# Kernel optimization log

Hardware: AMD Instinct MI355X
Metric: run time of the kernel (lower is better)

## Reference

```python
import jax, jax.numpy as jnp
import numpy as np

N = 50000      # nodes
E = 400000     # edges
IN = 64        # in_channels
HID = 64       # hidden_channels
H = 4          # num_heads
LAT = 32       # latent_dim
NEG_SLOPE = 0.2


def setup_inputs() -> dict:
    key = jax.random.key(0)
    ks = jax.random.split(key, 20)
    w = lambda k, shape, s=0.05: (jax.random.normal(k, shape, jnp.float32) * s)
    inp = {
        'x': jax.random.normal(ks[0], (N, IN), jnp.float32),
        'edge_index': jax.random.randint(ks[1], (2, E), 0, N, dtype=jnp.int32),
        'batch': jnp.zeros((N,), jnp.int32),
        'eps': jax.random.normal(ks[2], (N, LAT), jnp.float32),
        # conv1: in -> HID per head, 4 heads, concat
        'W1': w(ks[3], (IN, H * HID)), 'a_src1': w(ks[4], (H, HID)), 'a_dst1': w(ks[5], (H, HID)), 'b1': jnp.zeros((H * HID,), jnp.float32),
        # conv2: H*HID -> HID per head, concat
        'W2': w(ks[6], (H * HID, H * HID)), 'a_src2': w(ks[7], (H, HID)), 'a_dst2': w(ks[8], (H, HID)), 'b2': jnp.zeros((H * HID,), jnp.float32),
        # conv_mu / conv_logvar: H*HID -> LAT, 1 head, no concat
        'Wmu': w(ks[9], (H * HID, LAT)), 'a_src_mu': w(ks[10], (1, LAT)), 'a_dst_mu': w(ks[11], (1, LAT)), 'b_mu': jnp.zeros((LAT,), jnp.float32),
        'Wlv': w(ks[12], (H * HID, LAT)), 'a_src_lv': w(ks[13], (1, LAT)), 'a_dst_lv': w(ks[14], (1, LAT)), 'b_lv': jnp.zeros((LAT,), jnp.float32),
        # decoder
        'W_fc': w(ks[15], (LAT, HID)), 'b_fc': jnp.zeros((HID,), jnp.float32),
        'W_node': w(ks[16], (HID, IN)), 'b_node': jnp.zeros((IN,), jnp.float32),
        'W_edge': w(ks[17], (HID, 1)), 'b_edge': jnp.zeros((1,), jnp.float32),
    }
    return inp


def gat_layer(x, W, a_src, a_dst, b, src, dst, concat):
    """PyG-style GATConv: gather -> leaky_relu score -> per-dst softmax -> scatter-add."""
    n = x.shape[0]
    heads, c = a_src.shape
    h = (x @ W).reshape(n, heads, c)                     # [N,H,C]
    s_src = jnp.einsum('nhc,hc->nh', h, a_src)           # [N,H]
    s_dst = jnp.einsum('nhc,hc->nh', h, a_dst)
    e = jax.nn.leaky_relu(s_src[src] + s_dst[dst], NEG_SLOPE)   # [E,H]
    m = jax.ops.segment_max(e, dst, num_segments=n)      # stable softmax per destination
    e = jnp.exp(e - m[dst])
    denom = jax.ops.segment_sum(e, dst, num_segments=n)
    alpha = e / (denom[dst] + 1e-16)                     # [E,H]
    out = jax.ops.segment_sum(alpha[:, :, None] * h[src], dst, num_segments=n)  # [N,H,C]
    out = out.reshape(n, heads * c) if concat else out.mean(axis=1)
    return out + b


def reference(x, edge_index, batch, eps,
              W1, a_src1, a_dst1, b1,
              W2, a_src2, a_dst2, b2,
              Wmu, a_src_mu, a_dst_mu, b_mu,
              Wlv, a_src_lv, a_dst_lv, b_lv,
              W_fc, b_fc, W_node, b_node, W_edge, b_edge):
    n = x.shape[0]
    src0, dst0 = edge_index[0], edge_index[1]
    loops = jnp.arange(n, dtype=edge_index.dtype)        # GATConv add_self_loops=True
    src = jnp.concatenate([src0, loops])
    dst = jnp.concatenate([dst0, loops])

    # encode
    h = jax.nn.relu(gat_layer(x, W1, a_src1, a_dst1, b1, src, dst, concat=True))
    h = jax.nn.relu(gat_layer(h, W2, a_src2, a_dst2, b2, src, dst, concat=True))
    mu = gat_layer(h, Wmu, a_src_mu, a_dst_mu, b_mu, src, dst, concat=False)
    logvar = gat_layer(h, Wlv, a_src_lv, a_dst_lv, b_lv, src, dst, concat=False)

    # reparameterize (eps supplied for determinism)
    z = mu + eps * jnp.exp(0.5 * logvar)

    # decode
    zd = jax.nn.relu(z @ W_fc + b_fc)                    # [N,HID]
    node_features = zd @ W_node + b_node                 # [N,IN]
    edge_feat = zd[src0] * zd[dst0]                      # [E,HID]
    edge_scores = (edge_feat @ W_edge + b_edge).squeeze(-1)  # [E]
    return (mu, logvar, z, node_features, edge_scores)
```

## Files before the change

kernel.cpp:

```cpp
#include <hip/hip_runtime.h>
#include <math.h>

#define NEG_SLOPE 0.2f
#define CAP 32

__device__ __forceinline__ float lky(float x){ return x > 0.f ? x : NEG_SLOPE * x; }

__device__ __forceinline__ unsigned short f2bf(float f){
  unsigned int u = __float_as_uint(f);
  unsigned int r = (u + 0x7fffu + ((u >> 16) & 1u)) >> 16;
  return (unsigned short)r;
}
__device__ __forceinline__ float bf2f(unsigned short s){
  return __uint_as_float(((unsigned int)s) << 16);
}
__device__ __forceinline__ void unp8(uint4 v, float* f){
  f[0]=__uint_as_float(v.x<<16); f[1]=__uint_as_float(v.x&0xffff0000u);
  f[2]=__uint_as_float(v.y<<16); f[3]=__uint_as_float(v.y&0xffff0000u);
  f[4]=__uint_as_float(v.z<<16); f[5]=__uint_as_float(v.z&0xffff0000u);
  f[6]=__uint_as_float(v.w<<16); f[7]=__uint_as_float(v.w&0xffff0000u);
}
__device__ __forceinline__ uint4 pack8(const float* o){
  uint4 v;
  v.x = (unsigned)f2bf(o[0]) | ((unsigned)f2bf(o[1])<<16);
  v.y = (unsigned)f2bf(o[2]) | ((unsigned)f2bf(o[3])<<16);
  v.z = (unsigned)f2bf(o[4]) | ((unsigned)f2bf(o[5])<<16);
  v.w = (unsigned)f2bf(o[6]) | ((unsigned)f2bf(o[7])<<16);
  return v;
}

typedef __bf16 bf16x8 __attribute__((ext_vector_type(8)));
typedef float  f32x4  __attribute__((ext_vector_type(4)));
typedef float  f32x2  __attribute__((ext_vector_type(2)));

__device__ __forceinline__ uint2 pk_fp8(const float* f){
  unsigned lo = 0u, hi = 0u;
  lo = __builtin_amdgcn_cvt_pk_fp8_f32(f[0], f[1], (int)lo, false);
  lo = __builtin_amdgcn_cvt_pk_fp8_f32(f[2], f[3], (int)lo, true);
  hi = __builtin_amdgcn_cvt_pk_fp8_f32(f[4], f[5], (int)hi, false);
  hi = __builtin_amdgcn_cvt_pk_fp8_f32(f[6], f[7], (int)hi, true);
  return make_uint2(lo, hi);
}
__device__ __forceinline__ unsigned pk_fp8x4(float f0, float f1, float f2, float f3){
  unsigned u = 0u;
  u = __builtin_amdgcn_cvt_pk_fp8_f32(f0, f1, (int)u, false);
  u = __builtin_amdgcn_cvt_pk_fp8_f32(f2, f3, (int)u, true);
  return u;
}
__device__ __forceinline__ void unpk_fp8(uint2 v, float* f){
  f32x2 a0 = __builtin_amdgcn_cvt_pk_f32_fp8((int)v.x, false);
  f32x2 a1 = __builtin_amdgcn_cvt_pk_f32_fp8((int)v.x, true);
  f32x2 a2 = __builtin_amdgcn_cvt_pk_f32_fp8((int)v.y, false);
  f32x2 a3 = __builtin_amdgcn_cvt_pk_f32_fp8((int)v.y, true);
  f[0]=a0[0]; f[1]=a0[1]; f[2]=a1[0]; f[3]=a1[1];
  f[4]=a2[0]; f[5]=a2[1]; f[6]=a3[0]; f[7]=a3[1];
}

__device__ __forceinline__ void pack_one(const float* Wa, const float* Wb,
                                         int K, int M, int Mhalf,
                                         unsigned short* out, int idx){
  if (idx >= K * M) return;
  int j = idx & 7;
  int l = (idx >> 3) & 63;
  int rest = idx >> 9;
  int KS = K >> 5;
  int s = rest % KS, gct = rest / KS;
  int col = gct * 16 + (l & 15);
  int k   = s * 32 + ((l >> 4) << 3) + j;
  float v;
  if (Wb == nullptr) v = Wa[(long)k * M + col];
  else v = (col < Mhalf) ? Wa[(long)k * Mhalf + col] : Wb[(long)k * Mhalf + (col - Mhalf)];
  out[idx] = f2bf(v);
}

__global__ __launch_bounds__(256) void mega_kernel(
    const int* __restrict__ srcA, const int* __restrict__ dstA,
    int* __restrict__ cnt, int* __restrict__ colv2d, int E, int nbE,
    const float* __restrict__ W1,  unsigned short* __restrict__ W1pk,
    const float* __restrict__ W2,  unsigned short* __restrict__ W2pk,
    const float* __restrict__ Wmu, const float* __restrict__ Wlv,
    unsigned short* __restrict__ Wmvpk,
    const float* __restrict__ Wfc, unsigned short* __restrict__ Wfcpk,
    const float* __restrict__ Wnd, unsigned short* __restrict__ Wndpk,
    const float* __restrict__ as1, const float* __restrict__ ad1,
    const float* __restrict__ x, unsigned short* __restrict__ xb,
    float* __restrict__ S1s, float* __restrict__ S1d, int n)
{
  int b = blockIdx.x, t = threadIdx.x;
  if (b < nbE){
    int e = b * 256 + t;
    if (e < E){
      int d = dstA[e];
      int pos = atomicAdd(&cnt[d], 1);
      if (pos < CAP) colv2d[(long)d * CAP + pos] = srcA[e];
    }
    return;
  }
  b -= nbE;
  if (b < 408){
    if (b < 64)       pack_one(W1, nullptr, 64, 256, 256, W1pk, b * 256 + t);
    else if (b < 320) pack_one(W2, nullptr, 256, 256, 256, W2pk, (b - 64) * 256 + t);
    else if (b < 384) pack_one(Wmu, Wlv, 256, 64, 32, Wmvpk, (b - 320) * 256 + t);
    else if (b < 392) pack_one(Wfc, nullptr, 32, 64, 64, Wfcpk, (b - 384) * 256 + t);
    else              pack_one(Wnd, nullptr, 64, 64, 64, Wndpk, (b - 392) * 256 + t);
    return;
  }
  b -= 408;
  __shared__ float PT[512];
  #pragma unroll
  for (int rep = 0; rep < 2; ++rep){
    int idx = t + rep * 256;
    int o = idx >> 6, k = idx & 63;
    int sd = o & 1, h = o >> 1;
    const float* av = sd ? ad1 : as1;
    float acc = 0.f;
    for (int c = 0; c < 64; ++c) acc += W1[k * 256 + h * 64 + c] * av[h * 64 + c];
    PT[idx] = acc;
  }

  long base64 = (long)b * 64;
  {
    const float4* xg = (const float4*)x;
    uint4* xw = (uint4*)xb;
    long lim = (long)n * 8;
    long g0 = base64 * 8;
    #pragma unroll
    for (int rep = 0; rep < 2; ++rep){
      long p = g0 + t + rep * 256;
      if (p < lim){
        float4 v0 = xg[2 * p], v1 = xg[2 * p + 1];
        uint4 o;
        o.x = (unsigned)f2bf(v0.x) | ((unsigned)f2bf(v0.y) << 16);
        o.y = (unsigned)f2bf(v0.z) | ((unsigned)f2bf(v0.w) << 16);
        o.z = (unsigned)f2bf(v1.x) | ((unsigned)f2bf(v1.y) << 16);
        o.w = (unsigned)f2bf(v1.z) | ((unsigned)f2bf(v1.w) << 16);
        xw[p] = o;
      }
    }
  }
  __syncthreads();

  {
    int r = t >> 2, kq = t & 3;
    long nid = base64 + r;
    float acc[8] = {0,0,0,0,0,0,0,0};
    if (nid < n){
      const float4* xr4 = (const float4*)(x + nid * 64 + kq * 16);
      #pragma unroll
      for (int j4 = 0; j4 < 4; ++j4){
        float4 v = xr4[j4];
        float vf[4] = {v.x, v.y, v.z, v.w};
        #pragma unroll
        for (int jj = 0; jj < 4; ++jj){
          int k = kq * 16 + j4 * 4 + jj;
          #pragma unroll
          for (int o = 0; o < 8; ++o) acc[o] += vf[jj] * PT[o * 64 + k];
        }
      }
    }
    #pragma unroll
    for (int o = 0; o < 8; ++o){
      acc[o] += __shfl_xor(acc[o], 1);
      acc[o] += __shfl_xor(acc[o], 2);
    }
    if (kq == 0 && nid < n){
      *(float4*)(S1s + nid * 4) = make_float4(acc[0], acc[2], acc[4], acc[6]);
      *(float4*)(S1d + nid * 4) = make_float4(acc[1], acc[3], acc[5], acc[7]);
    }
  }
}

__global__ __launch_bounds__(256) void aggx_kernel(
    const unsigned short* __restrict__ xb,
    const float* __restrict__ Ss, const float* __restrict__ Sd,
    const int* __restrict__ cnt, const int* __restrict__ colv2d,
    unsigned short* __restrict__ Xagg, int n)
{
  int wv = threadIdx.x >> 6, l = threadIdx.x & 63;
  int nid = blockIdx.x * 4 + wv;
  if (nid >= n) return;
  int slot = l >> 4;
  int cl = l & 15;
  float4 sdv = *(const float4*)(Sd + (long)nid * 4);
  const uint2* xb2 = (const uint2*)xb;
  float acc[4][4] = {};
  float sumw[4] = {0.f, 0.f, 0.f, 0.f};
  int c = cnt[nid]; if (c > CAP) c = CAP;
  long rb = (long)nid * CAP;
  for (int jj = slot; jj < c; jj += 4){
    int s = colv2d[rb + jj];
    float4 a = *(const float4*)(Ss + (long)s * 4);
    float wx = __expf(lky(a.x + sdv.x));
    float wy = __expf(lky(a.y + sdv.y));
    float wz = __expf(lky(a.z + sdv.z));
    float ww = __expf(lky(a.w + sdv.w));
    uint2 xv = xb2[(long)s * 16 + cl];
    float f0 = __uint_as_float(xv.x << 16);
    float f1 = __uint_as_float(xv.x & 0xffff0000u);
    float f2 = __uint_as_float(xv.y << 16);
    float f3 = __uint_as_float(xv.y & 0xffff0000u);
    acc[0][0] += wx*f0; acc[0][1] += wx*f1; acc[0][2] += wx*f2; acc[0][3] += wx*f3;
    acc[1][0] += wy*f0; acc[1][1] += wy*f1; acc[1][2] += wy*f2; acc[1][3] += wy*f3;
    acc[2][0] += wz*f0; acc[2][1] += wz*f1; acc[2][2] += wz*f2; acc[2][3] += wz*f3;
    acc[3][0] += ww*f0; acc[3][1] += ww*f1; acc[3][2] += ww*f2; acc[3][3] += ww*f3;
    sumw[0] += wx; sumw[1] += wy; sumw[2] += wz; sumw[3] += ww;
  }
  #pragma unroll
  for (int d = 16; d <= 32; d <<= 1){
    #pragma unroll
    for (int h = 0; h < 4; ++h){
      #pragma unroll
      for (int j = 0; j < 4; ++j) acc[h][j] += __shfl_xor(acc[h][j], d);
      sumw[h] += __shfl_xor(sumw[h], d);
    }
  }
  float4 ssv = *(const float4*)(Ss + (long)nid * 4);
  uint2 xv = xb2[(long)nid * 16 + cl];
  float f0 = __uint_as_float(xv.x << 16);
  float f1 = __uint_as_float(xv.x & 0xffff0000u);
  float f2 = __uint_as_float(xv.y << 16);
  float f3 = __uint_as_float(xv.y & 0xffff0000u);
  float wsh[4] = { __expf(lky(ssv.x + sdv.x)), __expf(lky(ssv.y + sdv.y)),
                   __expf(lky(ssv.z + sdv.z)), __expf(lky(ssv.w + sdv.w)) };
  if (l < 16){
    uint2* Xo = (uint2*)Xagg;
    #pragma unroll
    for (int h = 0; h < 4; ++h){
      float inv = 1.f / (sumw[h] + wsh[h] + 1e-16f);
      float o0 = (acc[h][0] + wsh[h] * f0) * inv;
      float o1 = (acc[h][1] + wsh[h] * f1) * inv;
      float o2 = (acc[h][2] + wsh[h] * f2) * inv;
      float o3 = (acc[h][3] + wsh[h] * f3) * inv;
      uint2 ov;
      ov.x = (unsigned)f2bf(o0) | ((unsigned)f2bf(o1) << 16);
      ov.y = (unsigned)f2bf(o2) | ((unsigned)f2bf(o3) << 16);
      Xo[(long)nid * 64 + h * 16 + cl] = ov;
    }
  }
}

__global__ __launch_bounds__(256) void gemm12_kernel(
    const unsigned short* __restrict__ Xagg,
    const unsigned short* __restrict__ W1pk, const unsigned short* __restrict__ W2pk,
    const float* __restrict__ b1,
    const float* __restrict__ a_s, const float* __restrict__ a_d,
    unsigned char* __restrict__ H8,
    float* __restrict__ Ss, float* __restrict__ Sd, int n)
{
  constexpr int LDA = 264;
  __shared__ unsigned short As[32 * LDA];
  __shared__ unsigned short Bs[32 * LDA];
  const int t = threadIdx.x;
  const int w = t >> 6, l = t & 63;
  const int quad = l >> 4, l15 = l & 15;
  const long base = (long)blockIdx.x * 32;

  {
    const uint4* Xg = (const uint4*)Xagg;
    long g0 = base * 32;
    long lim = (long)n * 32;
    for (int c = t; c < 1024; c += 256){
      int row = c >> 5, kc = c & 31;
      uint4 v = make_uint4(0u, 0u, 0u, 0u);
      if (g0 + c < lim) v = Xg[g0 + c];
      *(uint4*)(As + row * LDA + kc * 8) = v;
    }
  }
  __syncthreads();

  f32x4 acc1[2][4] = {};
  const int abase = w * 64;
  #pragma unroll
  for (int s = 0; s < 2; ++s){
    bf16x8 af0 = *(const bf16x8*)(As + (0  + l15) * LDA + abase + s * 32 + quad * 8);
    bf16x8 af1 = *(const bf16x8*)(As + (16 + l15) * LDA + abase + s * 32 + quad * 8);
    #pragma unroll
    for (int ct = 0; ct < 4; ++ct){
      int gct = w * 4 + ct;
      bf16x8 bf = *(const bf16x8*)(W1pk + (((long)gct * 2 + s) * 64 + l) * 8);
      acc1[0][ct] = __builtin_amdgcn_mfma_f32_16x16x32_bf16(af0, bf, acc1[0][ct], 0, 0, 0);
      acc1[1][ct] = __builtin_amdgcn_mfma_f32_16x16x32_bf16(af1, bf, acc1[1][ct], 0, 0, 0);
    }
  }
  #pragma unroll
  for (int rt = 0; rt < 2; ++rt){
    #pragma unroll
    for (int ct = 0; ct < 4; ++ct){
      float b = b1[w * 64 + ct * 16 + l15];
      #pragma unroll
      for (int r = 0; r < 4; ++r){
        int row = rt * 16 + quad * 4 + r;
        Bs[row * LDA + w * 64 + ct * 16 + l15] = f2bf(fmaxf(acc1[rt][ct][r] + b, 0.f));
      }
    }
  }
  __syncthreads();

  f32x4 acc[2][4] = {};
  for (int s = 0; s < 8; ++s){
    bf16x8 af0 = *(const bf16x8*)(Bs + (0  + l15) * LDA + s * 32 + quad * 8);
    bf16x8 af1 = *(const bf16x8*)(Bs + (16 + l15) * LDA + s * 32 + quad * 8);
    #pragma unroll
    for (int ct = 0; ct < 4; ++ct){
      int gct = w * 4 + ct;
      bf16x8 bf = *(const bf16x8*)(W2pk + (((long)gct * 8 + s) * 64 + l) * 8);
      acc[0][ct] = __builtin_amdgcn_mfma_f32_16x16x32_bf16(af0, bf, acc[0][ct], 0, 0, 0);
      acc[1][ct] = __builtin_amdgcn_mfma_f32_16x16x32_bf16(af1, bf, acc[1][ct], 0, 0, 0);
    }
  }

  {
    float asv[4], adv[4];
    #pragma unroll
    for (int ct = 0; ct < 4; ++ct){
      int col = w * 64 + ct * 16 + l15;
      asv[ct] = a_s[col]; adv[ct] = a_d[col];
    }
    #pragma unroll
    for (int rt = 0; rt < 2; ++rt){
      #pragma unroll
      for (int r = 0; r < 4; ++r){
        float ps = 0.f, pd = 0.f;
        #pragma unroll
        for (int ct = 0; ct < 4; ++ct){
          float v = acc[rt][ct][r];
          ps += v * asv[ct]; pd += v * adv[ct];
        }
        ps += __shfl_xor(ps, 8); pd += __shfl_xor(pd, 8);
        ps += __shfl_xor(ps, 4); pd += __shfl_xor(pd, 4);
        ps += __shfl_xor(ps, 2); pd += __shfl_xor(pd, 2);
        ps += __shfl_xor(ps, 1); pd += __shfl_xor(pd, 1);
        long node = base + rt * 16 + quad * 4 + r;
        if (l15 == 0 && node < n){ Ss[node * 4 + w] = ps; Sd[node * 4 + w] = pd; }
      }
    }
  }

  #pragma unroll
  for (int rt = 0; rt < 2; ++rt){
    #pragma unroll
    for (int ct = 0; ct < 4; ++ct){
      #pragma unroll
      for (int r = 0; r < 4; ++r){
        int row = rt * 16 + quad * 4 + r;
        As[row * 256 + w * 64 + ct * 16 + l15] = f2bf(acc[rt][ct][r]);
      }
    }
  }
  __syncthreads();
  {
    uint2* Hg = (uint2*)H8;
    for (int c = t; c < 1024; c += 256){
      int row = c >> 5;
      uint4 v = *(const uint4*)(As + c * 8);
      float f[8]; unp8(v, f);
      if (base + row < n) Hg[base * 32 + c] = pk_fp8(f);
    }
  }
}

__global__ __launch_bounds__(256) void agg256_kernel(
    const unsigned char* __restrict__ H8,
    const float* __restrict__ Ss, const float* __restrict__ Sd,
    const int* __restrict__ cnt, const int* __restrict__ colv2d,
    const float* __restrict__ bias, unsigned short* __restrict__ Out, int n)
{
  int wv = threadIdx.x >> 6, l = threadIdx.x & 63;
  int nid = blockIdx.x * 4 + wv;
  if (nid >= n) return;
  int slot = l >> 4;
  int cl = l & 15;
  int head = cl >> 2;
  float sdv = Sd[(long)nid * 4 + head];
  const uint4* H8v = (const uint4*)H8;
  float acc[16] = {0,0,0,0,0,0,0,0,0,0,0,0,0,0,0,0};
  float sumw = 0.f;
  int c = cnt[nid]; if (c > CAP) c = CAP;
  long rb = (long)nid * CAP;
  for (int jj = slot; jj < c; jj += 4){
    int s = colv2d[rb + jj];
    float wt = __expf(lky(Ss[(long)s * 4 + head] + sdv));
    uint4 hv = H8v[(long)s * 16 + cl];
    float xf[16];
    unpk_fp8(make_uint2(hv.x, hv.y), xf);
    unpk_fp8(make_uint2(hv.z, hv.w), xf + 8);
    #pragma unroll
    for (int j = 0; j < 16; ++j) acc[j] += wt * xf[j];
    sumw += wt;
  }
  #pragma unroll
  for (int d = 16; d <= 32; d <<= 1){
    #pragma unroll
    for (int j = 0; j < 16; ++j) acc[j] += __shfl_xor(acc[j], d);
    sumw += __shfl_xor(sumw, d);
  }
  float wself = __expf(lky(Ss[(long)nid * 4 + head] + sdv));
  uint4 hv = H8v[(long)nid * 16 + cl];
  float xf[16];
  unpk_fp8(make_uint2(hv.x, hv.y), xf);
  unpk_fp8(make_uint2(hv.z, hv.w), xf + 8);
  if (l < 16){
    float inv = 1.f / (sumw + wself + 1e-16f);
    float o[16];
    #pragma unroll
    for (int j = 0; j < 16; ++j){
      float b = bias[cl * 16 + j];
      o[j] = fmaxf((acc[j] + wself * xf[j]) * inv + b, 0.f);
    }
    uint4* Og = (uint4*)Out;
    Og[(long)nid * 32 + cl * 2]     = pack8(o);
    Og[(long)nid * 32 + cl * 2 + 1] = pack8(o + 8);
  }
}

template<int K, int KB, int CW, bool BD, bool SCORES, bool RELU, bool OUT8>
__global__ __launch_bounds__(256) void gemm_mfma_kernel(
    const unsigned short* __restrict__ Xb, const unsigned short* __restrict__ Wpk,
    const float* __restrict__ a_s, const float* __restrict__ a_d,
    const float* __restrict__ a_s2, const float* __restrict__ a_d2,
    const float* __restrict__ bias,
    void* __restrict__ Hout,
    float* __restrict__ Ss, float* __restrict__ Sd,
    float* __restrict__ Ss2, float* __restrict__ Sd2, int n)
{
  constexpr int BR  = (CW == 4) ? 32 : 128;
  constexpr int M   = 64 * CW;
  constexpr int KSB = KB / 32;
  constexpr int LDA = K + 8;
  constexpr int SH  = (BR * LDA > BR * M) ? BR * LDA : BR * M;
  __shared__ unsigned short As[SH];

  const int t = threadIdx.x;
  const int w = t >> 6, l = t & 63;
  const int quad = l >> 4, l15 = l & 15;
  const long base = (long)blockIdx.x * BR;
  const int roww = (CW == 4) ? 0 : w;
  const int colw = (CW == 4) ? w : 0;
  const int abase = BD ? w * KB : 0;

  {
    const uint4* Xg = (const uint4*)Xb;
    long g0 = base * (K / 8);
    long lim = (long)n * (K / 8);
    for (int c = t; c < BR * K / 8; c += 256){
      int row = c / (K / 8), kc = c % (K / 8);
      uint4 v = make_uint4(0u, 0u, 0u, 0u);
      if (g0 + c < lim) v = Xg[g0 + c];
      *(uint4*)(As + row * LDA + kc * 8) = v;
    }
  }
  __syncthreads();

  f32x4 acc[2][4] = {};
  for (int s = 0; s < KSB; ++s){
    bf16x8 af0 = *(const bf16x8*)(As + (roww * 32 + 0  + l15) * LDA + abase + s * 32 + quad * 8);
    bf16x8 af1 = *(const bf16x8*)(As + (roww * 32 + 16 + l15) * LDA + abase + s * 32 + quad * 8);
    #pragma unroll
    for (int ct = 0; ct < 4; ++ct){
      int gct = colw * 4 + ct;
      bf16x8 bf = *(const bf16x8*)(Wpk + (((long)gct * KSB + s) * 64 + l) * 8);
      acc[0][ct] = __builtin_amdgcn_mfma_f32_16x16x32_bf16(af0, bf, acc[0][ct], 0, 0, 0);
      acc[1][ct] = __builtin_amdgcn_mfma_f32_16x16x32_bf16(af1, bf, acc[1][ct], 0, 0, 0);
    }
  }

  if constexpr (SCORES){
    float asm_[2], adm_[2], asl_[2], adl_[2];
    #pragma unroll
    for (int ct = 0; ct < 2; ++ct){
      int col = ct * 16 + l15;
      asm_[ct] = a_s[col];  adm_[ct] = a_d[col];
      asl_[ct] = a_s2[col]; adl_[ct] = a_d2[col];
    }
    #pragma unroll
    for (int rt = 0; rt < 2; ++rt){
      #pragma unroll
      for (int r = 0; r < 4; ++r){
        float psm = 0.f, pdm = 0.f, psl = 0.f, pdl = 0.f;
        #pragma unroll
        for (int ct = 0; ct < 2; ++ct){
          float vm = acc[rt][ct][r];
          float vl = acc[rt][ct + 2][r];
          psm += vm * asm_[ct]; pdm += vm * adm_[ct];
          psl += vl * asl_[ct]; pdl += vl * adl_[ct];
        }
        #pragma unroll
        for (int d = 8; d >= 1; d >>= 1){
          psm += __shfl_xor(psm, d); pdm += __shfl_xor(pdm, d);
          psl += __shfl_xor(psl, d); pdl += __shfl_xor(pdl, d);
        }
        long node = base + w * 32 + rt * 16 + quad * 4 + r;
        if (l15 == 0 && node < n){
          Ss[node]  = psm; Sd[node]  = pdm;
          Ss2[node] = psl; Sd2[node] = pdl;
        }
      }
    }
  }

  __syncthreads();
  #pragma unroll
  for (int rt = 0; rt < 2; ++rt){
    #pragma unroll
    for (int ct = 0; ct < 4; ++ct){
      #pragma unroll
      for (int r = 0; r < 4; ++r){
        int row = roww * 32 + rt * 16 + quad * 4 + r;
        int col = colw * 64 + ct * 16 + l15;
        float o = acc[rt][ct][r];
        int pos = col;
        if constexpr (CW == 1){ pos = (col < 32) ? (col * 2) : ((col - 32) * 2 + 1); }
        As[row * M + pos] = f2bf(o);
      }
    }
  }
  __syncthreads();
  {
    uint4* Hg = (uint4*)Hout;
    for (int c = t; c < BR * M / 8; c += 256){
      int row = c / (M / 8);
      if (base + row < n) Hg[base * (M / 8) + c] = *(const uint4*)(As + c * 8);
    }
  }
}

__global__ __launch_bounds__(256) void agg_muv_kernel(
    const unsigned short* __restrict__ Hmuv,
    const float* __restrict__ Ssm, const float* __restrict__ Sdm,
    const float* __restrict__ Ssl, const float* __restrict__ Sdl,
    const int* __restrict__ cnt, const int* __restrict__ colv2d,
    const float* __restrict__ bmu, const float* __restrict__ blv,
    const float* __restrict__ epsv,
    float* __restrict__ out_mu, float* __restrict__ out_lv, float* __restrict__ out_z,
    unsigned short* __restrict__ zb, int n)
{
  int wv = threadIdx.x >> 6, l = threadIdx.x & 63;
  int nid = blockIdx.x * 4 + wv;
  if (nid >= n) return;
  int slot = l >> 4;
  int cl = l & 15;
  float sdm = Sdm[nid], sdl = Sdl[nid];
  const uint2* Hm2 = (const uint2*)Hmuv;
  float am0 = 0.f, al0 = 0.f, am1 = 0.f, al1 = 0.f, summ = 0.f, suml = 0.f;
  int c = cnt[nid]; if (c > CAP) c = CAP;
  long rb = (long)nid * CAP;
  for (int jj = slot; jj < c; jj += 4){
    int s = colv2d[rb + jj];
    float wm = __expf(lky(Ssm[s] + sdm));
    float wl = __expf(lky(Ssl[s] + sdl));
    uint2 hv = Hm2[(long)s * 16 + cl];
    am0 += wm * __uint_as_float(hv.x << 16);
    al0 += wl * __uint_as_float(hv.x & 0xffff0000u);
    am1 += wm * __uint_as_float(hv.y << 16);
    al1 += wl * __uint_as_float(hv.y & 0xffff0000u);
    summ += wm; suml += wl;
  }
  #pragma unroll
  for (int d = 16; d <= 32; d <<= 1){
    am0 += __shfl_xor(am0, d); al0 += __shfl_xor(al0, d);
    am1 += __shfl_xor(am1, d); al1 += __shfl_xor(al1, d);
    summ += __shfl_xor(summ, d); suml += __shfl_xor(suml, d);
  }
  float wms = __expf(lky(Ssm[nid] + sdm));
  float wls = __expf(lky(Ssl[nid] + sdl));
  uint2 hv = Hm2[(long)nid * 16 + cl];
  float mus0 = __uint_as_float(hv.x << 16);
  float lvs0 = __uint_as_float(hv.x & 0xffff0000u);
  float mus1 = __uint_as_float(hv.y << 16);
  float lvs1 = __uint_as_float(hv.y & 0xffff0000u);
  if (l < 16){
    int c0 = cl * 2;
    float invm = 1.f / (summ + wms + 1e-16f);
    float invl = 1.f / (suml + wls + 1e-16f);
    float mu0 = (am0 + wms * mus0) * invm + bmu[c0];
    float lv0 = (al0 + wls * lvs0) * invl + blv[c0];
    float mu1 = (am1 + wms * mus1) * invm + bmu[c0 + 1];
    float lv1 = (al1 + wls * lvs1) * invl + blv[c0 + 1];
    float2 ev = *(const float2*)(epsv + (long)nid * 32 + c0);
    float z0 = mu0 + ev.x * expf(0.5f * lv0);
    float z1 = mu1 + ev.y * expf(0.5f * lv1);
    *(float2*)(out_mu + (long)nid * 32 + c0) = make_float2(mu0, mu1);
    *(float2*)(out_lv + (long)nid * 32 + c0) = make_float2(lv0, lv1);
    *(float2*)(out_z  + (long)nid * 32 + c0) = make_float2(z0, z1);
    *((unsigned*)zb + (long)nid * 16 + cl) = (unsigned)f2bf(z0) | ((unsigned)f2bf(z1) << 16);
  }
}

__global__ __launch_bounds__(256) void decoder_mfma_kernel(
    const unsigned short* __restrict__ zb,
    const unsigned short* __restrict__ Wfcpk, const float* __restrict__ bfc,
    const unsigned short* __restrict__ Wndpk, const float* __restrict__ bnode,
    unsigned char* __restrict__ ZD8, float* __restrict__ NF, int n)
{
  constexpr int LDA = 40;
  constexpr int LDZ = 72;
  __shared__ unsigned short As[128 * LDA];
  __shared__ unsigned short Zs[128 * LDZ];
  const int t = threadIdx.x;
  const int w = t >> 6, l = t & 63;
  const int quad = l >> 4, l15 = l & 15;
  const long base = (long)blockIdx.x * 128;

  {
    const uint4* Zg = (const uint4*)zb;
    long g0 = base * 4;
    long lim = (long)n * 4;
    for (int c = t; c < 512; c += 256){
      int row = c >> 2, kc = c & 3;
      uint4 v = make_uint4(0u, 0u, 0u, 0u);
      if (g0 + c < lim) v = Zg[g0 + c];
      *(uint4*)(As + row * LDA + kc * 8) = v;
    }
  }
  __syncthreads();

  f32x4 acc[2][4] = {};
  {
    bf16x8 af0 = *(const bf16x8*)(As + (w * 32 + 0  + l15) * LDA + quad * 8);
    bf16x8 af1 = *(const bf16x8*)(As + (w * 32 + 16 + l15) * LDA + quad * 8);
    #pragma unroll
    for (int ct = 0; ct < 4; ++ct){
      bf16x8 bf = *(const bf16x8*)(Wfcpk + (((long)ct) * 64 + l) * 8);
      acc[0][ct] = __builtin_amdgcn_mfma_f32_16x16x32_bf16(af0, bf, acc[0][ct], 0, 0, 0);
      acc[1][ct] = __builtin_amdgcn_mfma_f32_16x16x32_bf16(af1, bf, acc[1][ct], 0, 0, 0);
    }
  }
  #pragma unroll
  for (int rt = 0; rt < 2; ++rt){
    #pragma unroll
    for (int ct = 0; ct < 4; ++ct){
      float b = bfc[ct * 16 + l15];
      #pragma unroll
      for (int r = 0; r < 4; ++r){
        int row = w * 32 + rt * 16 + quad * 4 + r;
        Zs[row * LDZ + ct * 16 + l15] = f2bf(fmaxf(acc[rt][ct][r] + b, 0.f));
      }
    }
  }
  __syncthreads();

  {
    unsigned* Zgo = (unsigned*)ZD8;
    for (int c = t; c < 2048; c += 256){
      int row = c >> 4, kc = c & 15;
      uint2 v = *(const uint2*)(Zs + row * LDZ + kc * 4);
      float f0 = __uint_as_float(v.x << 16);
      float f1 = __uint_as_float(v.x & 0xffff0000u);
      float f2 = __uint_as_float(v.y << 16);
      float f3 = __uint_as_float(v.y & 0xffff0000u);
      if (base + row < n) Zgo[base * 16 + c] = pk_fp8x4(f0, f1, f2, f3);
    }
  }

  f32x4 acc2[2][4] = {};
  #pragma unroll
  for (int s = 0; s < 2; ++s){
    bf16x8 af0 = *(const bf16x8*)(Zs + (w * 32 + 0  + l15) * LDZ + s * 32 + quad * 8);
    bf16x8 af1 = *(const bf16x8*)(Zs + (w * 32 + 16 + l15) * LDZ + s * 32 + quad * 8);
    #pragma unroll
    for (int ct = 0; ct < 4; ++ct){
      bf16x8 bf = *(const bf16x8*)(Wndpk + (((long)ct * 2 + s) * 64 + l) * 8);
      acc2[0][ct] = __builtin_amdgcn_mfma_f32_16x16x32_bf16(af0, bf, acc2[0][ct], 0, 0, 0);
      acc2[1][ct] = __builtin_amdgcn_mfma_f32_16x16x32_bf16(af1, bf, acc2[1][ct], 0, 0, 0);
    }
  }
  #pragma unroll
  for (int rt = 0; rt < 2; ++rt){
    #pragma unroll
    for (int ct = 0; ct < 4; ++ct){
      float b = bnode[ct * 16 + l15];
      #pragma unroll
      for (int r = 0; r < 4; ++r){
        long row = base + w * 32 + rt * 16 + quad * 4 + r;
        if (row < n) NF[row * 64 + ct * 16 + l15] = acc2[rt][ct][r] + b;
      }
    }
  }
}

__global__ __launch_bounds__(256) void edge_score_kernel(
    const unsigned char* __restrict__ ZD8, const int* __restrict__ src, const int* __restrict__ dst,
    const float* __restrict__ Wedge, const float* __restrict__ bedge,
    float* __restrict__ out_es, int E)
{
  int gid = blockIdx.x * 256 + threadIdx.x;
  int l = threadIdx.x & 63;
  int slot = l >> 3, chunk = l & 7;
  int e = (gid >> 6) * 8 + slot;
  float4 we0 = *(const float4*)(Wedge + chunk * 8);
  float4 we1 = *(const float4*)(Wedge + chunk * 8 + 4);
  float p = 0.f;
  if (e < E){
    int s = src[e], d = dst[e];
    uint2 zs_ = *((const uint2*)ZD8 + (long)s * 8 + chunk);
    uint2 zd_ = *((const uint2*)ZD8 + (long)d * 8 + chunk);
    float a[8], b[8]; unpk_fp8(zs_, a); unpk_fp8(zd_, b);
    p = a[0]*b[0]*we0.x + a[1]*b[1]*we0.y + a[2]*b[2]*we0.z + a[3]*b[3]*we0.w
      + a[4]*b[4]*we1.x + a[5]*b[5]*we1.y + a[6]*b[6]*we1.z + a[7]*b[7]*we1.w;
  }
  p += __shfl_xor(p, 1);
  p += __shfl_xor(p, 2);
  p += __shfl_xor(p, 4);
  if (chunk == 0 && e < E) out_es[e] = p + bedge[0];
}

extern "C" void kernel_launch(void* const* d_in, const int* in_sizes, int n_in,
                              void* d_out, int out_size, void* d_ws, size_t ws_size,
                              hipStream_t stream)
{
  const float* x     = (const float*)d_in[0];
  const int*   ei    = (const int*)  d_in[1];
  const float* epsv  = (const float*)d_in[3];
  const float* W1    = (const float*)d_in[4];
  const float* as1   = (const float*)d_in[5];
  const float* ad1   = (const float*)d_in[6];
  const float* b1    = (const float*)d_in[7];
  const float* W2    = (const float*)d_in[8];
  const float* as2   = (const float*)d_in[9];
  const float* ad2   = (const float*)d_in[10];
  const float* b2    = (const float*)d_in[11];
  const float* Wmu   = (const float*)d_in[12];
  const float* asmu  = (const float*)d_in[13];
  const float* admu  = (const float*)d_in[14];
  const float* bmu   = (const float*)d_in[15];
  const float* Wlv   = (const float*)d_in[16];
  const float* aslv  = (const float*)d_in[17];
  const float* adlv  = (const float*)d_in[18];
  const float* blv   = (const float*)d_in[19];
  const float* Wfc   = (const float*)d_in[20];
  const float* bfc   = (const float*)d_in[21];
  const float* Wnode = (const float*)d_in[22];
  const float* bnode = (const float*)d_in[23];
  const float* Wedge = (const float*)d_in[24];
  const float* bedge = (const float*)d_in[25];

  const int N = in_sizes[0] / 64;
  const int E = in_sizes[1] / 2;
  const int* srcA = ei;
  const int* dstA = ei + E;

  char* wsb = (char*)d_ws;
  size_t off = 0;
  auto alloc = [&](size_t bytes) -> void* {
    void* p = wsb + off;
    off += (bytes + 255) & ~(size_t)255;
    return p;
  };
  unsigned short* xb    = (unsigned short*)alloc((size_t)N * 64 * 2);
  unsigned short* bufP  = (unsigned short*)alloc((size_t)N * 256 * 2);
  unsigned char*  H8    = (unsigned char*) alloc((size_t)N * 256);
  unsigned short* Hmuv  = (unsigned short*)alloc((size_t)N * 64 * 2);
  unsigned char*  ZD8   = (unsigned char*) alloc((size_t)N * 64);
  unsigned short* zbb   = (unsigned short*)alloc((size_t)N * 32 * 2);
  unsigned short* W1pk  = (unsigned short*)alloc((size_t)64 * 256 * 2);
  unsigned short* W2pk  = (unsigned short*)alloc((size_t)256 * 256 * 2);
  unsigned short* Wmvpk = (unsigned short*)alloc((size_t)256 * 64 * 2);
  unsigned short* Wfcpk = (unsigned short*)alloc((size_t)32 * 64 * 2);
  unsigned short* Wndpk = (unsigned short*)alloc((size_t)64 * 64 * 2);
  float* S1s   = (float*)alloc((size_t)N * 4 * 4);
  float* S1d   = (float*)alloc((size_t)N * 4 * 4);
  float* S2s   = (float*)alloc((size_t)N * 4 * 4);
  float* S2d   = (float*)alloc((size_t)N * 4 * 4);
  float* Ssm   = (float*)alloc((size_t)N * 4);
  float* Sdm   = (float*)alloc((size_t)N * 4);
  float* Ssl   = (float*)alloc((size_t)N * 4);
  float* Sdl   = (float*)alloc((size_t)N * 4);
  int*   cnt   = (int*)  alloc((size_t)N * 4);
  int*   colv2d= (int*)  alloc((size_t)N * CAP * 4);
  (void)ws_size; (void)n_in; (void)out_size;

  float* out_mu = (float*)d_out;
  float* out_lv = out_mu + (size_t)N * 32;
  float* out_z  = out_lv + (size_t)N * 32;
  float* out_nf = out_z  + (size_t)N * 32;
  float* out_es = out_nf + (size_t)N * 64;

  const int nb64 = (N + 63) / 64;
  const int nbE  = (E + 255) / 256;

  hipMemsetAsync(cnt, 0, (size_t)N * 4, stream);
  mega_kernel<<<nbE + 408 + nb64, 256, 0, stream>>>(
      srcA, dstA, cnt, colv2d, E, nbE,
      W1, W1pk, W2, W2pk, Wmu, Wlv, Wmvpk, Wfc, Wfcpk, Wnode, Wndpk,
      as1, ad1, x, xb, S1s, S1d, N);

  aggx_kernel<<<(N + 3) / 4, 256, 0, stream>>>(xb, S1s, S1d, cnt, colv2d, bufP, N);
  gemm12_kernel<<<(N + 31) / 32, 256, 0, stream>>>(
      bufP, W1pk, W2pk, b1, as2, ad2, H8, S2s, S2d, N);
  agg256_kernel<<<(N + 3) / 4, 256, 0, stream>>>(H8, S2s, S2d, cnt, colv2d, b2, bufP, N);

  gemm_mfma_kernel<256, 256, 1, false, true, false, false><<<(N + 127) / 128, 256, 0, stream>>>(
      bufP, Wmvpk, asmu, admu, aslv, adlv, nullptr, Hmuv,
      Ssm, Sdm, Ssl, Sdl, N);
  agg_muv_kernel<<<(N + 3) / 4, 256, 0, stream>>>(
      Hmuv, Ssm, Sdm, Ssl, Sdl, cnt, colv2d, bmu, blv, epsv,
      out_mu, out_lv, out_z, zbb, N);

  decoder_mfma_kernel<<<(N + 127) / 128, 256, 0, stream>>>(
      zbb, Wfcpk, bfc, Wndpk, bnode, ZD8, out_nf, N);
  {
    long waves = ((long)E + 7) / 8;
    long blocks = (waves + 3) / 4;
    edge_score_kernel<<<(int)blocks, 256, 0, stream>>>(ZD8, srcA, dstA, Wedge, bedge, out_es, E);
  }
}
```

Baseline: 313.9 us.

## Fuse layer-1 attention aggregation into gemm12 and interleave mu/logvar scores

```diff
diff --git a/kernel.cpp b/kernel.cpp
--- a/kernel.cpp
+++ b/kernel.cpp
@@ -170,77 +170,10 @@
   }
 }
 
-__global__ __launch_bounds__(256) void aggx_kernel(
+__global__ __launch_bounds__(256) void gemm12_kernel(
     const unsigned short* __restrict__ xb,
-    const float* __restrict__ Ss, const float* __restrict__ Sd,
+    const float* __restrict__ S1s, const float* __restrict__ S1d,
     const int* __restrict__ cnt, const int* __restrict__ colv2d,
-    unsigned short* __restrict__ Xagg, int n)
-{
-  int wv = threadIdx.x >> 6, l = threadIdx.x & 63;
-  int nid = blockIdx.x * 4 + wv;
-  if (nid >= n) return;
-  int slot = l >> 4;
-  int cl = l & 15;
-  float4 sdv = *(const float4*)(Sd + (long)nid * 4);
-  const uint2* xb2 = (const uint2*)xb;
-  float acc[4][4] = {};
-  float sumw[4] = {0.f, 0.f, 0.f, 0.f};
-  int c = cnt[nid]; if (c > CAP) c = CAP;
-  long rb = (long)nid * CAP;
-  for (int jj = slot; jj < c; jj += 4){
-    int s = colv2d[rb + jj];
-    float4 a = *(const float4*)(Ss + (long)s * 4);
-    float wx = __expf(lky(a.x + sdv.x));
-    float wy = __expf(lky(a.y + sdv.y));
-    float wz = __expf(lky(a.z + sdv.z));
-    float ww = __expf(lky(a.w + sdv.w));
-    uint2 xv = xb2[(long)s * 16 + cl];
-    float f0 = __uint_as_float(xv.x << 16);
-    float f1 = __uint_as_float(xv.x & 0xffff0000u);
-    float f2 = __uint_as_float(xv.y << 16);
-    float f3 = __uint_as_float(xv.y & 0xffff0000u);
-    acc[0][0] += wx*f0; acc[0][1] += wx*f1; acc[0][2] += wx*f2; acc[0][3] += wx*f3;
-    acc[1][0] += wy*f0; acc[1][1] += wy*f1; acc[1][2] += wy*f2; acc[1][3] += wy*f3;
-    acc[2][0] += wz*f0; acc[2][1] += wz*f1; acc[2][2] += wz*f2; acc[2][3] += wz*f3;
-    acc[3][0] += ww*f0; acc[3][1] += ww*f1; acc[3][2] += ww*f2; acc[3][3] += ww*f3;
-    sumw[0] += wx; sumw[1] += wy; sumw[2] += wz; sumw[3] += ww;
-  }
-  #pragma unroll
-  for (int d = 16; d <= 32; d <<= 1){
-    #pragma unroll
-    for (int h = 0; h < 4; ++h){
-      #pragma unroll
-      for (int j = 0; j < 4; ++j) acc[h][j] += __shfl_xor(acc[h][j], d);
-      sumw[h] += __shfl_xor(sumw[h], d);
-    }
-  }
-  float4 ssv = *(const float4*)(Ss + (long)nid * 4);
-  uint2 xv = xb2[(long)nid * 16 + cl];
-  float f0 = __uint_as_float(xv.x << 16);
-  float f1 = __uint_as_float(xv.x & 0xffff0000u);
-  float f2 = __uint_as_float(xv.y << 16);
-  float f3 = __uint_as_float(xv.y & 0xffff0000u);
-  float wsh[4] = { __expf(lky(ssv.x + sdv.x)), __expf(lky(ssv.y + sdv.y)),
-                   __expf(lky(ssv.z + sdv.z)), __expf(lky(ssv.w + sdv.w)) };
-  if (l < 16){
-    uint2* Xo = (uint2*)Xagg;
-    #pragma unroll
-    for (int h = 0; h < 4; ++h){
-      float inv = 1.f / (sumw[h] + wsh[h] + 1e-16f);
-      float o0 = (acc[h][0] + wsh[h] * f0) * inv;
-      float o1 = (acc[h][1] + wsh[h] * f1) * inv;
-      float o2 = (acc[h][2] + wsh[h] * f2) * inv;
-      float o3 = (acc[h][3] + wsh[h] * f3) * inv;
-      uint2 ov;
-      ov.x = (unsigned)f2bf(o0) | ((unsigned)f2bf(o1) << 16);
-      ov.y = (unsigned)f2bf(o2) | ((unsigned)f2bf(o3) << 16);
-      Xo[(long)nid * 64 + h * 16 + cl] = ov;
-    }
-  }
-}
-
-__global__ __launch_bounds__(256) void gemm12_kernel(
-    const unsigned short* __restrict__ Xagg,
     const unsigned short* __restrict__ W1pk, const unsigned short* __restrict__ W2pk,
     const float* __restrict__ b1,
     const float* __restrict__ a_s, const float* __restrict__ a_d,
@@ -256,14 +189,66 @@
   const long base = (long)blockIdx.x * 32;
 
   {
-    const uint4* Xg = (const uint4*)Xagg;
-    long g0 = base * 32;
-    long lim = (long)n * 32;
-    for (int c = t; c < 1024; c += 256){
-      int row = c >> 5, kc = c & 31;
-      uint4 v = make_uint4(0u, 0u, 0u, 0u);
-      if (g0 + c < lim) v = Xg[g0 + c];
-      *(uint4*)(As + row * LDA + kc * 8) = v;
+    const int slot = l >> 4, cl = l & 15;
+    const uint2* xb2 = (const uint2*)xb;
+    for (int nx = 0; nx < 8; ++nx){
+      int row = w * 8 + nx;
+      long nid = base + row;
+      if (nid >= n) continue;
+      float4 sdv = *(const float4*)(S1d + nid * 4);
+      float acc[4][4] = {};
+      float sumw[4] = {0.f, 0.f, 0.f, 0.f};
+      int c = cnt[nid]; if (c > CAP) c = CAP;
+      long rb = nid * CAP;
+      for (int jj = slot; jj < c; jj += 4){
+        int s = colv2d[rb + jj];
+        float4 a = *(const float4*)(S1s + (long)s * 4);
+        float wx = __expf(lky(a.x + sdv.x));
+        float wy = __expf(lky(a.y + sdv.y));
+        float wz = __expf(lky(a.z + sdv.z));
+        float ww = __expf(lky(a.w + sdv.w));
+        uint2 xv = xb2[(long)s * 16 + cl];
+        float f0 = __uint_as_float(xv.x << 16);
+        float f1 = __uint_as_float(xv.x & 0xffff0000u);
+        float f2 = __uint_as_float(xv.y << 16);
+        float f3 = __uint_as_float(xv.y & 0xffff0000u);
+        acc[0][0] += wx*f0; acc[0][1] += wx*f1; acc[0][2] += wx*f2; acc[0][3] += wx*f3;
+        acc[1][0] += wy*f0; acc[1][1] += wy*f1; acc[1][2] += wy*f2; acc[1][3] += wy*f3;
+        acc[2][0] += wz*f0; acc[2][1] += wz*f1; acc[2][2] += wz*f2; acc[2][3] += wz*f3;
+        acc[3][0] += ww*f0; acc[3][1] += ww*f1; acc[3][2] += ww*f2; acc[3][3] += ww*f3;
+        sumw[0] += wx; sumw[1] += wy; sumw[2] += wz; sumw[3] += ww;
+      }
+      #pragma unroll
+      for (int d = 16; d <= 32; d <<= 1){
+        #pragma unroll
+        for (int h = 0; h < 4; ++h){
+          #pragma unroll
+          for (int j = 0; j < 4; ++j) acc[h][j] += __shfl_xor(acc[h][j], d);
+          sumw[h] += __shfl_xor(sumw[h], d);
+        }
+      }
+      float4 ssv = *(const float4*)(S1s + nid * 4);
+      uint2 xv = xb2[nid * 16 + cl];
+      float f0 = __uint_as_float(xv.x << 16);
+      float f1 = __uint_as_float(xv.x & 0xffff0000u);
+      float f2 = __uint_as_float(xv.y << 16);
+      float f3 = __uint_as_float(xv.y & 0xffff0000u);
+      float wsh[4] = { __expf(lky(ssv.x + sdv.x)), __expf(lky(ssv.y + sdv.y)),
+                       __expf(lky(ssv.z + sdv.z)), __expf(lky(ssv.w + sdv.w)) };
+      if (l < 16){
+        #pragma unroll
+        for (int h = 0; h < 4; ++h){
+          float inv = 1.f / (sumw[h] + wsh[h] + 1e-16f);
+          float o0 = (acc[h][0] + wsh[h] * f0) * inv;
+          float o1 = (acc[h][1] + wsh[h] * f1) * inv;
+          float o2 = (acc[h][2] + wsh[h] * f2) * inv;
+          float o3 = (acc[h][3] + wsh[h] * f3) * inv;
+          uint2 ov;
+          ov.x = (unsigned)f2bf(o0) | ((unsigned)f2bf(o1) << 16);
+          ov.y = (unsigned)f2bf(o2) | ((unsigned)f2bf(o3) << 16);
+          *(uint2*)(As + row * LDA + (h * 16 + cl) * 4) = ov;
+        }
+      }
     }
   }
   __syncthreads();
@@ -491,8 +476,8 @@
         }
         long node = base + w * 32 + rt * 16 + quad * 4 + r;
         if (l15 == 0 && node < n){
-          Ss[node]  = psm; Sd[node]  = pdm;
-          Ss2[node] = psl; Sd2[node] = pdl;
+          ((float2*)Ss)[node] = make_float2(psm, psl);
+          ((float2*)Sd)[node] = make_float2(pdm, pdl);
         }
       }
     }
@@ -526,8 +511,7 @@
 
 __global__ __launch_bounds__(256) void agg_muv_kernel(
     const unsigned short* __restrict__ Hmuv,
-    const float* __restrict__ Ssm, const float* __restrict__ Sdm,
-    const float* __restrict__ Ssl, const float* __restrict__ Sdl,
+    const float* __restrict__ SsML, const float* __restrict__ SdML,
     const int* __restrict__ cnt, const int* __restrict__ colv2d,
     const float* __restrict__ bmu, const float* __restrict__ blv,
     const float* __restrict__ epsv,
@@ -539,15 +523,16 @@
   if (nid >= n) return;
   int slot = l >> 4;
   int cl = l & 15;
-  float sdm = Sdm[nid], sdl = Sdl[nid];
+  float2 dML = ((const float2*)SdML)[nid];
   const uint2* Hm2 = (const uint2*)Hmuv;
   float am0 = 0.f, al0 = 0.f, am1 = 0.f, al1 = 0.f, summ = 0.f, suml = 0.f;
   int c = cnt[nid]; if (c > CAP) c = CAP;
   long rb = (long)nid * CAP;
   for (int jj = slot; jj < c; jj += 4){
     int s = colv2d[rb + jj];
-    float wm = __expf(lky(Ssm[s] + sdm));
-    float wl = __expf(lky(Ssl[s] + sdl));
+    float2 sML = ((const float2*)SsML)[s];
+    float wm = __expf(lky(sML.x + dML.x));
+    float wl = __expf(lky(sML.y + dML.y));
     uint2 hv = Hm2[(long)s * 16 + cl];
     am0 += wm * __uint_as_float(hv.x << 16);
     al0 += wl * __uint_as_float(hv.x & 0xffff0000u);
@@ -561,8 +546,9 @@
     am1 += __shfl_xor(am1, d); al1 += __shfl_xor(al1, d);
     summ += __shfl_xor(summ, d); suml += __shfl_xor(suml, d);
   }
-  float wms = __expf(lky(Ssm[nid] + sdm));
-  float wls = __expf(lky(Ssl[nid] + sdl));
+  float2 selfML = ((const float2*)SsML)[nid];
+  float wms = __expf(lky(selfML.x + dML.x));
+  float wls = __expf(lky(selfML.y + dML.y));
   uint2 hv = Hm2[(long)nid * 16 + cl];
   float mus0 = __uint_as_float(hv.x << 16);
   float lvs0 = __uint_as_float(hv.x & 0xffff0000u);
@@ -761,10 +747,8 @@
   float* S1d   = (float*)alloc((size_t)N * 4 * 4);
   float* S2s   = (float*)alloc((size_t)N * 4 * 4);
   float* S2d   = (float*)alloc((size_t)N * 4 * 4);
-  float* Ssm   = (float*)alloc((size_t)N * 4);
-  float* Sdm   = (float*)alloc((size_t)N * 4);
-  float* Ssl   = (float*)alloc((size_t)N * 4);
-  float* Sdl   = (float*)alloc((size_t)N * 4);
+  float* SsML  = (float*)alloc((size_t)N * 8);
+  float* SdML  = (float*)alloc((size_t)N * 8);
   int*   cnt   = (int*)  alloc((size_t)N * 4);
   int*   colv2d= (int*)  alloc((size_t)N * CAP * 4);
   (void)ws_size; (void)n_in; (void)out_size;
@@ -784,16 +768,15 @@
       W1, W1pk, W2, W2pk, Wmu, Wlv, Wmvpk, Wfc, Wfcpk, Wnode, Wndpk,
       as1, ad1, x, xb, S1s, S1d, N);
 
-  aggx_kernel<<<(N + 3) / 4, 256, 0, stream>>>(xb, S1s, S1d, cnt, colv2d, bufP, N);
   gemm12_kernel<<<(N + 31) / 32, 256, 0, stream>>>(
-      bufP, W1pk, W2pk, b1, as2, ad2, H8, S2s, S2d, N);
+      xb, S1s, S1d, cnt, colv2d, W1pk, W2pk, b1, as2, ad2, H8, S2s, S2d, N);
   agg256_kernel<<<(N + 3) / 4, 256, 0, stream>>>(H8, S2s, S2d, cnt, colv2d, b2, bufP, N);
 
   gemm_mfma_kernel<256, 256, 1, false, true, false, false><<<(N + 127) / 128, 256, 0, stream>>>(
       bufP, Wmvpk, asmu, admu, aslv, adlv, nullptr, Hmuv,
-      Ssm, Sdm, Ssl, Sdl, N);
+      SsML, SdML, nullptr, nullptr, N);
   agg_muv_kernel<<<(N + 3) / 4, 256, 0, stream>>>(
-      Hmuv, Ssm, Sdm, Ssl, Sdl, cnt, colv2d, bmu, blv, epsv,
+      Hmuv, SsML, SdML, cnt, colv2d, bmu, blv, epsv,
       out_mu, out_lv, out_z, zbb, N);
 
   decoder_mfma_kernel<<<(N + 127) / 128, 256, 0, stream>>>(
```

Result: slower. 322.2 us (+2.7%).
